# Kernel tuning notes

Measured on AMD Instinct MI355X. Metric: run time of the kernel, lower is better.

Reference implementation:

```python
import jax, jax.numpy as jnp
import numpy as np

N_NODES = 100000
N_EDGES = 1638400
IN_FEAT = 128
OUT_FEAT = 64
NUM_RELS = 8


def setup_inputs() -> dict:
    key = jax.random.key(0)
    k1, k2, k3, k4, k5 = jax.random.split(key, 5)
    feat = jax.random.normal(k1, (N_NODES, IN_FEAT), dtype=jnp.float32)
    W = jax.random.normal(k2, (NUM_RELS, OUT_FEAT, IN_FEAT), dtype=jnp.float32) * 0.05
    edge_src = jax.random.randint(k3, (N_EDGES,), 0, N_NODES, dtype=jnp.int32)
    edge_dst = jax.random.randint(k4, (N_EDGES,), 0, N_NODES, dtype=jnp.int32)
    edge_type = jax.random.randint(k5, (N_EDGES,), 0, NUM_RELS, dtype=jnp.int32)
    return {"feat": feat, "W": W, "edge_src": edge_src,
            "edge_dst": edge_dst, "edge_type": edge_type}


def reference(feat, W, edge_src, edge_dst, edge_type):
    # RGCN hetero forward: Y[i,fo] = sum_{edges e: dst(e)=i} W[rel(e)] @ feat[src(e)]
    # Transform all node features under every relation once: [R, N, out].
    xw = jnp.einsum('nf,rof->rno', feat, W)
    # Per-edge message gather: [E, out]
    msg = xw[edge_type, edge_src]
    # Scatter-add into destination nodes: [N, out]
    y = jax.ops.segment_sum(msg, edge_dst, num_segments=feat.shape[0])
    return y
```

## Files before the change

kernel.cpp:

```cpp
#include <hip/hip_runtime.h>
#include <hip/hip_bf16.h>
#include <stdint.h>

#define N_NODES 100000
#define N_EDGES 1638400
#define IN_FEAT 128
#define OUT_FEAT 64
#define NUM_RELS 8
#define NTILES ((N_NODES + 63) / 64)
#define TGRID 1024

#define BUCKET_BITS 9
#define BUCKET_SIZE 512
#define NBUCKETS ((N_NODES + BUCKET_SIZE - 1) / BUCKET_SIZE)
#define ABLOCKS 200
#define AEDGES (N_EDGES / ABLOCKS)
#define APT (AEDGES / 1024)
#define BK 12

typedef __attribute__((ext_vector_type(8))) short short8;
typedef __attribute__((ext_vector_type(4))) short short4v;
typedef __attribute__((ext_vector_type(4))) float floatx4;

__device__ __forceinline__ unsigned short f2bf(float x) {
    union { float f; uint32_t u; } c; c.f = x;
    uint32_t u = c.u;
    u += 0x7FFFu + ((u >> 16) & 1u);
    return (unsigned short)(u >> 16);
}

__device__ __forceinline__ uint32_t cvt_pk_bf16(float lo, float hi) {
    uint32_t r;
    asm("v_cvt_pk_bf16_f32 %0, %1, %2" : "=v"(r) : "v"(lo), "v"(hi));
    return r;
}

#define W8 (NUM_RELS * OUT_FEAT * IN_FEAT / 8)
__global__ __launch_bounds__(256)
void prep_kernel(const float* __restrict__ W, unsigned short* __restrict__ W_bf,
                 int* __restrict__ bucketHist) {
    int u = blockIdx.x * 256 + threadIdx.x;
    if (u < NBUCKETS) bucketHist[u] = 0;
    int w = u - NBUCKETS;
    if (w >= 0 && w < W8) {
        const float* s = W + (size_t)w * 8;
        float4 a = *(const float4*)s, b = *(const float4*)(s + 4);
        short8 v;
        v[0] = f2bf(a.x); v[1] = f2bf(a.y); v[2] = f2bf(a.z); v[3] = f2bf(a.w);
        v[4] = f2bf(b.x); v[5] = f2bf(b.y); v[6] = f2bf(b.z); v[7] = f2bf(b.w);
        *(short8*)(W_bf + (size_t)w * 8) = v;
    }
}

__global__ __launch_bounds__(1024)
void buckethist_kernel(const int* __restrict__ dst, int* __restrict__ bucketHist) {
    __shared__ int h[NBUCKETS];
    const int t = threadIdx.x;
    if (t < NBUCKETS) h[t] = 0;
    __syncthreads();
    #pragma unroll
    for (int i = 0; i < APT; ++i) {
        int e = blockIdx.x * AEDGES + i * 1024 + t;
        atomicAdd(&h[dst[e] >> BUCKET_BITS], 1);
    }
    __syncthreads();
    if (t < NBUCKETS && h[t] > 0) atomicAdd(&bucketHist[t], h[t]);
}

__global__ __launch_bounds__(256)
void bucketscan_kernel(const int* __restrict__ bucketHist, int* __restrict__ bucketStart,
                       int* __restrict__ bucketCursor) {
    __shared__ int wtot[4];
    const int t = threadIdx.x, lane = t & 63, wv = t >> 6;
    int v = (t < NBUCKETS) ? bucketHist[t] : 0;
    int x = v;
    #pragma unroll
    for (int d = 1; d < 64; d <<= 1) {
        int tv = __shfl_up(x, d, 64);
        if (lane >= d) x += tv;
    }
    if (lane == 63) wtot[wv] = x;
    __syncthreads();
    if (t == 0) {
        int run = 0;
        #pragma unroll
        for (int j = 0; j < 4; ++j) { int c = wtot[j]; wtot[j] = run; run += c; }
    }
    __syncthreads();
    int excl = x - v + wtot[wv];
    if (t < NBUCKETS) { bucketStart[t] = excl; bucketCursor[t] = excl; }
    if (t == 0) bucketStart[NBUCKETS] = N_EDGES;
}

__global__ __launch_bounds__(1024)
void bin_kernel(const int* __restrict__ src, const int* __restrict__ dst,
                const int* __restrict__ typ, int* __restrict__ bucketCursor,
                uint32_t* __restrict__ bins) {
    __shared__ int h[NBUCKETS];
    __shared__ int base[NBUCKETS];
    const int t = threadIdx.x;
    if (t < NBUCKETS) h[t] = 0;
    __syncthreads();
    uint32_t pk[APT]; int bk[APT], rk[APT];
    #pragma unroll
    for (int i = 0; i < APT; ++i) {
        int e = blockIdx.x * AEDGES + i * 1024 + t;
        int d = dst[e];
        int b = d >> BUCKET_BITS;
        bk[i] = b;
        pk[i] = ((uint32_t)(d & (BUCKET_SIZE - 1)) << 20) | ((uint32_t)typ[e] << 17) | (uint32_t)src[e];
        rk[i] = atomicAdd(&h[b], 1);
    }
    __syncthreads();
    if (t < NBUCKETS && h[t] > 0) base[t] = atomicAdd(&bucketCursor[t], h[t]);
    __syncthreads();
    #pragma unroll
    for (int i = 0; i < APT; ++i)
        bins[base[bk[i]] + rk[i]] = pk[i];
}

__global__ __launch_bounds__(1024)
void sortb_kernel(const int* __restrict__ bucketStart, uint32_t* __restrict__ bins,
                  int* __restrict__ offs) {
    __shared__ int cnt_l[BUCKET_SIZE];
    __shared__ int start_l[BUCKET_SIZE];
    __shared__ int wtot[8];
    const int b = blockIdx.x;
    const int t = threadIdx.x, lane = t & 63, wv = t >> 6;
    const int s = bucketStart[b];
    const int cnt = bucketStart[b + 1] - s;
    if (t < BUCKET_SIZE) cnt_l[t] = 0;
    __syncthreads();
    uint32_t pk[BK]; int rk[BK], ld[BK];
    #pragma unroll
    for (int k = 0; k < BK; ++k) {
        int idx = t + k * 1024;
        ld[k] = -1;
        if (idx < cnt) {
            uint32_t p = bins[s + idx];
            pk[k] = p;
            ld[k] = (int)(p >> 20);
            rk[k] = atomicAdd(&cnt_l[ld[k]], 1);
        }
    }
    __syncthreads();
    int v = 0, x = 0;
    if (t < BUCKET_SIZE) {
        v = cnt_l[t]; x = v;
        #pragma unroll
        for (int d = 1; d < 64; d <<= 1) {
            int tv = __shfl_up(x, d, 64);
            if (lane >= d) x += tv;
        }
        if (lane == 63) wtot[wv] = x;
    }
    __syncthreads();
    if (t == 0) {
        int run = 0;
        #pragma unroll
        for (int j = 0; j < 8; ++j) { int c = wtot[j]; wtot[j] = run; run += c; }
    }
    __syncthreads();
    if (t < BUCKET_SIZE) {
        int excl = x - v + wtot[wv];
        start_l[t] = excl;
        int node = b * BUCKET_SIZE + t;
        if (node < N_NODES) offs[node] = ((s + excl) << 8) | v;
    }
    __syncthreads();
    #pragma unroll
    for (int k = 0; k < BK; ++k)
        if (ld[k] >= 0)
            bins[s + start_l[ld[k]] + rk[k]] = pk[k];
}

__global__ __launch_bounds__(512)
void transform_kernel(const float* __restrict__ feat,
                      const unsigned short* __restrict__ W_bf,
                      unsigned short* __restrict__ xw) {
    const int t    = threadIdx.x;
    const int lane = t & 63;
    const int r    = t >> 6;
    const int quad = lane >> 4;
    const int lrow = lane & 15;

    __shared__ unsigned short sA[2][64 * 136];

    short8 wfr[4][4];
    #pragma unroll
    for (int jm = 0; jm < 4; ++jm)
        #pragma unroll
        for (int kk = 0; kk < 4; ++kk)
            wfr[jm][kk] = *(const short8*)(W_bf +
                ((size_t)r * OUT_FEAT + jm * 16 + lrow) * IN_FEAT + kk * 32 + quad * 8);

    int tile = blockIdx.x;

    #pragma unroll
    for (int i = 0; i < 4; ++i) {
        int f4 = t + 512 * i;
        int row = f4 >> 5, c4 = f4 & 31;
        int n = tile * 64 + row;
        float4 v = (n < N_NODES) ? *(const float4*)(feat + (size_t)n * IN_FEAT + c4 * 4)
                                 : make_float4(0.f, 0.f, 0.f, 0.f);
        uint2 q;
        q.x = cvt_pk_bf16(v.x, v.y);
        q.y = cvt_pk_bf16(v.z, v.w);
        *(uint2*)&sA[0][row * 136 + c4 * 4] = q;
    }

    int p = 0;
    while (tile < NTILES) {
        __syncthreads();
        const int nxt = tile + TGRID;
        const bool have_nxt = (nxt < NTILES);

        float4 ra[4];
        if (have_nxt) {
            #pragma unroll
            for (int i = 0; i < 4; ++i) {
                int f4 = t + 512 * i;
                int row = f4 >> 5, c4 = f4 & 31;
                int n = nxt * 64 + row;
                ra[i] = (n < N_NODES) ? *(const float4*)(feat + (size_t)n * IN_FEAT + c4 * 4)
                                      : make_float4(0.f, 0.f, 0.f, 0.f);
            }
        }

        const int n0 = tile * 64;
        const bool full = (n0 + 64 <= N_NODES);
        #pragma unroll
        for (int nb = 0; nb < 4; ++nb) {
            floatx4 acc[4] = {{0,0,0,0},{0,0,0,0},{0,0,0,0},{0,0,0,0}};
            #pragma unroll
            for (int kk = 0; kk < 4; ++kk) {
                short8 bfrag = *(const short8*)&sA[p][(nb * 16 + lrow) * 136 + kk * 32 + quad * 8];
                #pragma unroll
                for (int jm = 0; jm < 4; ++jm)
                    acc[jm] = __builtin_amdgcn_mfma_f32_16x16x32_bf16(wfr[jm][kk], bfrag, acc[jm], 0, 0, 0);
            }
            int n = n0 + nb * 16 + lrow;
            if (full || n < N_NODES) {
                unsigned short* rowp = xw + ((size_t)r * N_NODES + n) * OUT_FEAT;
                #pragma unroll
                for (int jm = 0; jm < 4; ++jm) {
                    uint2 u;
                    u.x = (uint32_t)f2bf(acc[jm][0]) | ((uint32_t)f2bf(acc[jm][1]) << 16);
                    u.y = (uint32_t)f2bf(acc[jm][2]) | ((uint32_t)f2bf(acc[jm][3]) << 16);
                    *(uint2*)(rowp + jm * 16 + quad * 4) = u;
                }
            }
        }

        if (have_nxt) {
            #pragma unroll
            for (int i = 0; i < 4; ++i) {
                int f4 = t + 512 * i;
                int row = f4 >> 5, c4 = f4 & 31;
                uint2 q;
                q.x = cvt_pk_bf16(ra[i].x, ra[i].y);
                q.y = cvt_pk_bf16(ra[i].z, ra[i].w);
                *(uint2*)&sA[p ^ 1][row * 136 + c4 * 4] = q;
            }
        }
        p ^= 1;
        tile = nxt;
    }
}

__global__ __launch_bounds__(256)
void gather_kernel(const unsigned short* __restrict__ xw, const int* __restrict__ offs,
                   const uint32_t* __restrict__ bins, float* __restrict__ out) {
    const int wv = threadIdx.x >> 6;
    const int lane = threadIdx.x & 63;
    const int g = lane >> 3;
    const int l = lane & 7;
    const int node = blockIdx.x * 4 + wv;
    if (node >= N_NODES) return;
    const int pd = offs[node];
    const int start = pd >> 8;
    const int deg = pd & 255;
    float acc[8] = {0.f, 0.f, 0.f, 0.f, 0.f, 0.f, 0.f, 0.f};
    for (int base = 0; base < deg; base += 64) {
        int rem = deg - base; if (rem > 64) rem = 64;
        uint32_t pl = bins[start + base + lane];
        int rounds = (rem + 7) >> 3;
        for (int i = 0; i < rounds; ++i) {
            int ei = i * 8 + g;
            uint32_t p = __shfl(pl, ei, 64);
            if (ei < rem) {
                int rel = (p >> 17) & 7;
                int src = (int)(p & 0x1FFFF);
                const uint4* q = (const uint4*)(xw + ((size_t)rel * N_NODES + src) * OUT_FEAT + l * 8);
                uint4 u = *q;
                union { uint32_t u; float f; } c;
                c.u = u.x << 16;         acc[0] += c.f;
                c.u = u.x & 0xFFFF0000u; acc[1] += c.f;
                c.u = u.y << 16;         acc[2] += c.f;
                c.u = u.y & 0xFFFF0000u; acc[3] += c.f;
                c.u = u.z << 16;         acc[4] += c.f;
                c.u = u.z & 0xFFFF0000u; acc[5] += c.f;
                c.u = u.w << 16;         acc[6] += c.f;
                c.u = u.w & 0xFFFF0000u; acc[7] += c.f;
            }
        }
    }
    #pragma unroll
    for (int d = 8; d < 64; d <<= 1) {
        #pragma unroll
        for (int j = 0; j < 8; ++j)
            acc[j] += __shfl_xor(acc[j], d, 64);
    }
    if (g == 0) {
        float* rowp = out + (size_t)node * OUT_FEAT + l * 8;
        float4 a = make_float4(acc[0], acc[1], acc[2], acc[3]);
        float4 b = make_float4(acc[4], acc[5], acc[6], acc[7]);
        *(float4*)rowp = a;
        *(float4*)(rowp + 4) = b;
    }
}

extern "C" void kernel_launch(void* const* d_in, const int* in_sizes, int n_in,
                              void* d_out, int out_size, void* d_ws, size_t ws_size,
                              hipStream_t stream) {
    const float* feat = (const float*)d_in[0];
    const float* W    = (const float*)d_in[1];
    const int* esrc   = (const int*)d_in[2];
    const int* edst   = (const int*)d_in[3];
    const int* etyp   = (const int*)d_in[4];
    float* out = (float*)d_out;

    char* ws = (char*)d_ws;
    size_t ofs = 0;
    unsigned short* xw = (unsigned short*)(ws + ofs);
    ofs += (size_t)NUM_RELS * N_NODES * OUT_FEAT * 2;
    unsigned short* W_bf = (unsigned short*)(ws + ofs);
    ofs += (size_t)NUM_RELS * OUT_FEAT * IN_FEAT * 2;
    uint32_t* bins = (uint32_t*)(ws + ofs);
    ofs += (size_t)N_EDGES * 4 + 256;
    int* offs = (int*)(ws + ofs);
    ofs += ((size_t)N_NODES * 4 + 255) & ~(size_t)255;
    int* bucketHist = (int*)(ws + ofs);   ofs += 1024;
    int* bucketStart = (int*)(ws + ofs);  ofs += 1024;
    int* bucketCursor = (int*)(ws + ofs); ofs += 1024;

    prep_kernel<<<(NBUCKETS + W8 + 255) / 256, 256, 0, stream>>>(W, W_bf, bucketHist);
    buckethist_kernel<<<ABLOCKS, 1024, 0, stream>>>(edst, bucketHist);
    bucketscan_kernel<<<1, 256, 0, stream>>>(bucketHist, bucketStart, bucketCursor);
    bin_kernel<<<ABLOCKS, 1024, 0, stream>>>(esrc, edst, etyp, bucketCursor, bins);
    sortb_kernel<<<NBUCKETS, 1024, 0, stream>>>(bucketStart, bins, offs);
    transform_kernel<<<TGRID, 512, 0, stream>>>(feat, W_bf, xw);
    gather_kernel<<<(N_NODES + 3) / 4, 256, 0, stream>>>(xw, offs, bins, out);
}
```

Before: 138.2 us.

## Fuse edge binning and feature transform into one heterogeneous-block launch

Merges the edge bin-scatter kernel and the node feature transform kernel into a single launch. The first 400 blocks do edge binning with 512 threads each, and the remaining 1024 blocks run the MFMA transform. The aim is to overlap the two independent phases and save one kernel launch. The transform prefetch is also changed to convert and store the next tile into LDS immediately rather than holding it in registers. This lowers register pressure but exposes load latency before the compute, and the binning blocks now reserve the transform's LDS footprint.

```diff
diff --git a/kernel.cpp b/kernel.cpp
--- a/kernel.cpp
+++ b/kernel.cpp
@@ -16,10 +16,12 @@
 #define ABLOCKS 200
 #define AEDGES (N_EDGES / ABLOCKS)
 #define APT (AEDGES / 1024)
+#define BINB 400
+#define BEDGES (N_EDGES / BINB)
+#define BPT (BEDGES / 512)
 #define BK 12
 
 typedef __attribute__((ext_vector_type(8))) short short8;
-typedef __attribute__((ext_vector_type(4))) short short4v;
 typedef __attribute__((ext_vector_type(4))) float floatx4;
 
 __device__ __forceinline__ unsigned short f2bf(float x) {
@@ -92,100 +94,46 @@
     if (t == 0) bucketStart[NBUCKETS] = N_EDGES;
 }
 
-__global__ __launch_bounds__(1024)
-void bin_kernel(const int* __restrict__ src, const int* __restrict__ dst,
-                const int* __restrict__ typ, int* __restrict__ bucketCursor,
-                uint32_t* __restrict__ bins) {
+__global__ __launch_bounds__(512)
+void fused_bin_transform_kernel(const int* __restrict__ src, const int* __restrict__ dst,
+                                const int* __restrict__ typ, int* __restrict__ bucketCursor,
+                                uint32_t* __restrict__ bins,
+                                const float* __restrict__ feat,
+                                const unsigned short* __restrict__ W_bf,
+                                unsigned short* __restrict__ xw) {
+    __shared__ unsigned short sA[2][64 * 136];
     __shared__ int h[NBUCKETS];
     __shared__ int base[NBUCKETS];
-    const int t = threadIdx.x;
-    if (t < NBUCKETS) h[t] = 0;
-    __syncthreads();
-    uint32_t pk[APT]; int bk[APT], rk[APT];
-    #pragma unroll
-    for (int i = 0; i < APT; ++i) {
-        int e = blockIdx.x * AEDGES + i * 1024 + t;
-        int d = dst[e];
-        int b = d >> BUCKET_BITS;
-        bk[i] = b;
-        pk[i] = ((uint32_t)(d & (BUCKET_SIZE - 1)) << 20) | ((uint32_t)typ[e] << 17) | (uint32_t)src[e];
-        rk[i] = atomicAdd(&h[b], 1);
-    }
-    __syncthreads();
-    if (t < NBUCKETS && h[t] > 0) base[t] = atomicAdd(&bucketCursor[t], h[t]);
-    __syncthreads();
-    #pragma unroll
-    for (int i = 0; i < APT; ++i)
-        bins[base[bk[i]] + rk[i]] = pk[i];
-}
-
-__global__ __launch_bounds__(1024)
-void sortb_kernel(const int* __restrict__ bucketStart, uint32_t* __restrict__ bins,
-                  int* __restrict__ offs) {
-    __shared__ int cnt_l[BUCKET_SIZE];
-    __shared__ int start_l[BUCKET_SIZE];
-    __shared__ int wtot[8];
-    const int b = blockIdx.x;
-    const int t = threadIdx.x, lane = t & 63, wv = t >> 6;
-    const int s = bucketStart[b];
-    const int cnt = bucketStart[b + 1] - s;
-    if (t < BUCKET_SIZE) cnt_l[t] = 0;
-    __syncthreads();
-    uint32_t pk[BK]; int rk[BK], ld[BK];
-    #pragma unroll
-    for (int k = 0; k < BK; ++k) {
-        int idx = t + k * 1024;
-        ld[k] = -1;
-        if (idx < cnt) {
-            uint32_t p = bins[s + idx];
-            pk[k] = p;
-            ld[k] = (int)(p >> 20);
-            rk[k] = atomicAdd(&cnt_l[ld[k]], 1);
-        }
-    }
-    __syncthreads();
-    int v = 0, x = 0;
-    if (t < BUCKET_SIZE) {
-        v = cnt_l[t]; x = v;
-        #pragma unroll
-        for (int d = 1; d < 64; d <<= 1) {
-            int tv = __shfl_up(x, d, 64);
-            if (lane >= d) x += tv;
-        }
-        if (lane == 63) wtot[wv] = x;
-    }
-    __syncthreads();
-    if (t == 0) {
-        int run = 0;
-        #pragma unroll
-        for (int j = 0; j < 8; ++j) { int c = wtot[j]; wtot[j] = run; run += c; }
-    }
-    __syncthreads();
-    if (t < BUCKET_SIZE) {
-        int excl = x - v + wtot[wv];
-        start_l[t] = excl;
-        int node = b * BUCKET_SIZE + t;
-        if (node < N_NODES) offs[node] = ((s + excl) << 8) | v;
-    }
-    __syncthreads();
-    #pragma unroll
-    for (int k = 0; k < BK; ++k)
-        if (ld[k] >= 0)
-            bins[s + start_l[ld[k]] + rk[k]] = pk[k];
-}
-
-__global__ __launch_bounds__(512)
-void transform_kernel(const float* __restrict__ feat,
-                      const unsigned short* __restrict__ W_bf,
-                      unsigned short* __restrict__ xw) {
+
+    if (blockIdx.x < BINB) {
+        const int t = threadIdx.x;
+        if (t < NBUCKETS) h[t] = 0;
+        __syncthreads();
+        uint32_t pk[BPT]; int bk[BPT], rk[BPT];
+        #pragma unroll
+        for (int i = 0; i < BPT; ++i) {
+            int e = blockIdx.x * BEDGES + i * 512 + t;
+            int d = dst[e];
+            int b = d >> BUCKET_BITS;
+            bk[i] = b;
+            pk[i] = ((uint32_t)(d & (BUCKET_SIZE - 1)) << 20) | ((uint32_t)typ[e] << 17) | (uint32_t)src[e];
+            rk[i] = atomicAdd(&h[b], 1);
+        }
+        __syncthreads();
+        if (t < NBUCKETS && h[t] > 0) base[t] = atomicAdd(&bucketCursor[t], h[t]);
+        __syncthreads();
+        #pragma unroll
+        for (int i = 0; i < BPT; ++i)
+            bins[base[bk[i]] + rk[i]] = pk[i];
+        return;
+    }
+
     const int t    = threadIdx.x;
     const int lane = t & 63;
     const int r    = t >> 6;
     const int quad = lane >> 4;
     const int lrow = lane & 15;
 
-    __shared__ unsigned short sA[2][64 * 136];
-
     short8 wfr[4][4];
     #pragma unroll
     for (int jm = 0; jm < 4; ++jm)
@@ -194,7 +142,7 @@
             wfr[jm][kk] = *(const short8*)(W_bf +
                 ((size_t)r * OUT_FEAT + jm * 16 + lrow) * IN_FEAT + kk * 32 + quad * 8);
 
-    int tile = blockIdx.x;
+    int tile = blockIdx.x - BINB;
 
     #pragma unroll
     for (int i = 0; i < 4; ++i) {
@@ -212,18 +160,19 @@
     int p = 0;
     while (tile < NTILES) {
         __syncthreads();
-        const int nxt = tile + TGRID;
-        const bool have_nxt = (nxt < NTILES);
-
-        float4 ra[4];
-        if (have_nxt) {
+        int nxt = tile + TGRID;
+        if (nxt < NTILES) {
             #pragma unroll
             for (int i = 0; i < 4; ++i) {
                 int f4 = t + 512 * i;
                 int row = f4 >> 5, c4 = f4 & 31;
                 int n = nxt * 64 + row;
-                ra[i] = (n < N_NODES) ? *(const float4*)(feat + (size_t)n * IN_FEAT + c4 * 4)
-                                      : make_float4(0.f, 0.f, 0.f, 0.f);
+                float4 v = (n < N_NODES) ? *(const float4*)(feat + (size_t)n * IN_FEAT + c4 * 4)
+                                         : make_float4(0.f, 0.f, 0.f, 0.f);
+                uint2 q;
+                q.x = cvt_pk_bf16(v.x, v.y);
+                q.y = cvt_pk_bf16(v.z, v.w);
+                *(uint2*)&sA[p ^ 1][row * 136 + c4 * 4] = q;
             }
         }
 
@@ -251,21 +200,64 @@
                 }
             }
         }
-
-        if (have_nxt) {
-            #pragma unroll
-            for (int i = 0; i < 4; ++i) {
-                int f4 = t + 512 * i;
-                int row = f4 >> 5, c4 = f4 & 31;
-                uint2 q;
-                q.x = cvt_pk_bf16(ra[i].x, ra[i].y);
-                q.y = cvt_pk_bf16(ra[i].z, ra[i].w);
-                *(uint2*)&sA[p ^ 1][row * 136 + c4 * 4] = q;
-            }
-        }
         p ^= 1;
         tile = nxt;
     }
+}
+
+__global__ __launch_bounds__(1024)
+void sortb_kernel(const int* __restrict__ bucketStart, uint32_t* __restrict__ bins,
+                  int* __restrict__ offs) {
+    __shared__ int cnt_l[BUCKET_SIZE];
+    __shared__ int start_l[BUCKET_SIZE];
+    __shared__ int wtot[8];
+    const int b = blockIdx.x;
+    const int t = threadIdx.x, lane = t & 63, wv = t >> 6;
+    const int s = bucketStart[b];
+    const int cnt = bucketStart[b + 1] - s;
+    if (t < BUCKET_SIZE) cnt_l[t] = 0;
+    __syncthreads();
+    uint32_t pk[BK]; int rk[BK], ld[BK];
+    #pragma unroll
+    for (int k = 0; k < BK; ++k) {
+        int idx = t + k * 1024;
+        ld[k] = -1;
+        if (idx < cnt) {
+            uint32_t p = bins[s + idx];
+            pk[k] = p;
+            ld[k] = (int)(p >> 20);
+            rk[k] = atomicAdd(&cnt_l[ld[k]], 1);
+        }
+    }
+    __syncthreads();
+    int v = 0, x = 0;
+    if (t < BUCKET_SIZE) {
+        v = cnt_l[t]; x = v;
+        #pragma unroll
+        for (int d = 1; d < 64; d <<= 1) {
+            int tv = __shfl_up(x, d, 64);
+            if (lane >= d) x += tv;
+        }
+        if (lane == 63) wtot[wv] = x;
+    }
+    __syncthreads();
+    if (t == 0) {
+        int run = 0;
+        #pragma unroll
+        for (int j = 0; j < 8; ++j) { int c = wtot[j]; wtot[j] = run; run += c; }
+    }
+    __syncthreads();
+    if (t < BUCKET_SIZE) {
+        int excl = x - v + wtot[wv];
+        start_l[t] = excl;
+        int node = b * BUCKET_SIZE + t;
+        if (node < N_NODES) offs[node] = ((s + excl) << 8) | v;
+    }
+    __syncthreads();
+    #pragma unroll
+    for (int k = 0; k < BK; ++k)
+        if (ld[k] >= 0)
+            bins[s + start_l[ld[k]] + rk[k]] = pk[k];
 }
 
 __global__ __launch_bounds__(256)
@@ -347,8 +339,8 @@
     prep_kernel<<<(NBUCKETS + W8 + 255) / 256, 256, 0, stream>>>(W, W_bf, bucketHist);
     buckethist_kernel<<<ABLOCKS, 1024, 0, stream>>>(edst, bucketHist);
     bucketscan_kernel<<<1, 256, 0, stream>>>(bucketHist, bucketStart, bucketCursor);
-    bin_kernel<<<ABLOCKS, 1024, 0, stream>>>(esrc, edst, etyp, bucketCursor, bins);
+    fused_bin_transform_kernel<<<BINB + TGRID, 512, 0, stream>>>(
+        esrc, edst, etyp, bucketCursor, bins, feat, W_bf, xw);
     sortb_kernel<<<NBUCKETS, 1024, 0, stream>>>(bucketStart, bins, offs);
-    transform_kernel<<<TGRID, 512, 0, stream>>>(feat, W_bf, xw);
     gather_kernel<<<(N_NODES + 3) / 4, 256, 0, stream>>>(xw, offs, bins, out);
 }
```

After: 130.8 us. -5.4%, faster.
